# Performance work log

Measured on AMD Instinct MI355X. Metric: run time of the kernel, lower is better.

The kernel has to match this reference:

```python
import jax, jax.numpy as jnp
import numpy as np
from math import sqrt

S, B = 512, 64
V, E, H, T = 50000, 256, 512, 9
PAD = 0

def setup_inputs() -> dict:
    key = jax.random.key(0)
    ks = jax.random.split(key, 12)
    x = jax.random.randint(ks[0], (S, B), 0, V)
    x = x.at[0].set(jnp.maximum(x[0], 1))  # first token never pad (CRF mask req)
    bio = jax.random.randint(ks[1], (S, B), 0, T)
    sc = 0.02
    return {
        "x": x, "bio": bio,
        "emb": jax.random.normal(ks[2], (V, E), jnp.float32) * sc,
        "W_ih": jax.random.normal(ks[3], (4 * H, E), jnp.float32) * sc,
        "W_hh": jax.random.normal(ks[4], (4 * H, H), jnp.float32) * sc,
        "b_ih": jnp.zeros((4 * H,), jnp.float32),
        "b_hh": jnp.zeros((4 * H,), jnp.float32),
        "W_out": jax.random.normal(ks[5], (T, H), jnp.float32) * sc,
        "b_out": jnp.zeros((T,), jnp.float32),
        "start_t": jax.random.normal(ks[6], (T,), jnp.float32) * 0.1,
        "end_t": jax.random.normal(ks[7], (T,), jnp.float32) * 0.1,
        "trans": jax.random.normal(ks[8], (T, T), jnp.float32) * 0.1,
    }

def _lstm(embeds, W_ih, W_hh, b_ih, b_hh):
    # embeds: [S,B,E] time-major, single layer, pytorch gate order i,f,g,o
    def step(carry, e_t):
        h, c = carry
        gates = e_t @ W_ih.T + h @ W_hh.T + (b_ih + b_hh)  # [B,4H]
        i, f, g, o = jnp.split(gates, 4, axis=-1)
        i, f, o = jax.nn.sigmoid(i), jax.nn.sigmoid(f), jax.nn.sigmoid(o)
        c = f * c + i * jnp.tanh(g)
        h = o * jnp.tanh(c)
        return (h, c), h
    h0 = jnp.zeros((embeds.shape[1], W_hh.shape[1]), embeds.dtype)
    _, hs = jax.lax.scan(step, (h0, h0), embeds)
    return hs  # [S,B,H]

def _crf_llh(emissions, tags, maskf, start_t, end_t, trans):
    # emissions [S,B,T], tags [S,B], maskf [S,B] float. Returns summed log-likelihood.
    Bn = emissions.shape[1]
    barange = jnp.arange(Bn)
    em = jnp.take_along_axis(emissions, tags[:, :, None], axis=2)[:, :, 0]  # [S,B]
    tr = trans[tags[:-1], tags[1:]]  # [S-1,B]
    seq_ends = maskf.sum(0).astype(jnp.int32) - 1
    last_tags = tags[seq_ends, barange]
    num = (start_t[tags[0]] + em[0]
           + ((em[1:] + tr) * maskf[1:]).sum(0)
           + end_t[last_tags])  # [B]
    # normalizer: forward algorithm
    def step(score, inp):
        e_t, m_t = inp  # [B,T], [B]
        nxt = jax.nn.logsumexp(score[:, :, None] + trans[None] + e_t[:, None, :], axis=1)
        score = jnp.where(m_t[:, None] > 0, nxt, score)
        return score, None
    score0 = start_t[None] + emissions[0]  # [B,T]
    scoreN, _ = jax.lax.scan(step, score0, (emissions[1:], maskf[1:]))
    norm = jax.nn.logsumexp(scoreN + end_t[None], axis=1)  # [B]
    return (num - norm).sum()

def _viterbi(emissions, start_t, end_t, trans):
    # full-length decode (model calls crf.decode without mask)
    Bn, Tn = emissions.shape[1], emissions.shape[2]
    barange = jnp.arange(Bn)
    def step(score, e_t):
        cand = score[:, :, None] + trans[None]  # [B,T_prev,T_next]
        idx = jnp.argmax(cand, axis=1)          # [B,T]
        score = jnp.max(cand, axis=1) + e_t
        return score, idx
    score0 = start_t[None] + emissions[0]
    scoreN, history = jax.lax.scan(step, score0, emissions[1:])  # history [S-1,B,T]
    last = jnp.argmax(scoreN + end_t[None], axis=1)  # [B]
    def back(tag, h_t):
        prev = h_t[barange, tag]
        return prev, tag
    tag0, rest = jax.lax.scan(back, last, history, reverse=True)  # rest[t] = tag_{t+1}
    return jnp.concatenate([tag0[None], rest], axis=0)  # [S,B]

def reference(x, bio, emb, W_ih, W_hh, b_ih, b_hh, W_out, b_out, start_t, end_t, trans):
    maskf = (x != PAD).astype(jnp.float32)  # [S,B]
    embeds = emb[x] * sqrt(E)               # [S,B,E]
    lstm_out = _lstm(embeds, W_ih, W_hh, b_ih, b_hh)  # [S,B,H]
    logits = lstm_out @ W_out.T + b_out               # [S,B,T]
    emissions = jax.nn.log_softmax(logits, axis=-1)
    llh = _crf_llh(emissions, bio, maskf, start_t, end_t, trans)
    crf_tags = _viterbi(emissions, start_t, end_t, trans)
    return (-llh, crf_tags)
```

## Files before the change

kernel.cpp:

```cpp
#include <hip/hip_runtime.h>
#include <math.h>

#define SS 512
#define BB 64
#define EE 256
#define HH 512
#define NT 9
#define NWG 256

#define HS_ELEMS ((size_t)SS * BB * HH)
#define EM_OFF   HS_ELEMS
#define NUM_OFF  (EM_OFF + (size_t)SS * BB * NT)
#define NORM_OFF (NUM_OFF + 64)
#define FLAG_OFF (NORM_OFF + 64)
#define FLAG_U32S ((size_t)SS * 8 * 32)

#define L_WHH 0
#define L_H   32768
#define L_GSM 36928
#define L_CS  37504
#define L_TOT 37632

__global__ __launch_bounds__(256) void init_flags(float* __restrict__ ws) {
    unsigned* f = (unsigned*)(ws + FLAG_OFF);
    size_t idx = (size_t)blockIdx.x * 256 + threadIdx.x;
    if (idx < FLAG_U32S) f[idx] = 0u;
}

__global__ __launch_bounds__(512) void lstm_persistent(
    const float* __restrict__ Whh, const float* __restrict__ Wih,
    const float* __restrict__ bih, const float* __restrict__ bhh,
    const float* __restrict__ emb, const int* __restrict__ x,
    float* __restrict__ ws)
{
    const int wg    = blockIdx.x;
    const int slice = wg & 31;
    const int bg    = wg >> 5;
    const int tid   = threadIdx.x;
    const int w     = tid >> 6;
    const int L     = tid & 63;
    const int b_l   = L & 7;
    const int kc    = L >> 3;
    const int b     = bg * 8 + b_l;

    float* hs = ws;
    unsigned* flags = (unsigned*)(ws + FLAG_OFF);

    extern __shared__ float smem[];
    float* whh_l = smem + L_WHH;
    float* h_l   = smem + L_H;
    float* gsm   = smem + L_GSM;
    float* cs_l  = smem + L_CS;

    int grow[8];
#pragma unroll
    for (int r = 0; r < 8; r++) {
        int l = w * 8 + r;
        grow[r] = (l >> 4) * HH + slice * 16 + (l & 15);
    }

    for (int j = 0; j < 64; j++) {
        int idx = j * 512 + tid;
        int l = idx >> 9;
        int k = idx & 511;
        int gr = (l >> 4) * HH + slice * 16 + (l & 15);
        whh_l[idx] = Whh[(size_t)gr * HH + k];
    }

    float bs0 = 0.f, bs1 = 0.f, bs2 = 0.f, bs3 = 0.f;
    if (tid < 128) {
        const int u  = tid & 15;
        const int bb = tid >> 4;
        const int gu = slice * 16 + u;
        bs0 = bih[0 * HH + gu] + bhh[0 * HH + gu];
        bs1 = bih[1 * HH + gu] + bhh[1 * HH + gu];
        bs2 = bih[2 * HH + gu] + bhh[2 * HH + gu];
        bs3 = bih[3 * HH + gu] + bhh[3 * HH + gu];
        cs_l[u * 8 + bb] = 0.0f;
    }

#pragma unroll
    for (int j = 0; j < 8; j++) {
        int idx = j * 512 + tid;
        h_l[(idx >> 9) * 520 + (idx & 511)] = 0.0f;
    }

    float acc_ih[8];
    {
        const int xv = x[0 * BB + b];
        const float* erow = emb + (size_t)xv * EE;
#pragma unroll
        for (int r = 0; r < 8; r++) acc_ih[r] = 0.0f;
        for (int c = 0; c < 8; c++) {
            const int k0 = c * 32 + kc * 4;
            float4 e4 = *(const float4*)(erow + k0);
            e4.x *= 16.0f; e4.y *= 16.0f; e4.z *= 16.0f; e4.w *= 16.0f;
#pragma unroll
            for (int r = 0; r < 8; r++) {
                float4 w4 = *(const float4*)(Wih + (size_t)grow[r] * EE + k0);
                acc_ih[r] += w4.x * e4.x + w4.y * e4.y + w4.z * e4.z + w4.w * e4.w;
            }
        }
    }
    __syncthreads();

    const float* wbase = whh_l + (size_t)(w * 8) * 512;

    for (int t = 0; t < SS; t++) {
        float acc[8];
#pragma unroll
        for (int r = 0; r < 8; r++) acc[r] = acc_ih[r];
        const float* hrow = h_l + b_l * 520;
        for (int c = 0; c < 16; c++) {
            const int k0 = c * 32 + kc * 4;
            float4 h4 = *(const float4*)(hrow + k0);
#pragma unroll
            for (int r = 0; r < 8; r++) {
                float4 w4 = *(const float4*)(wbase + r * 512 + k0);
                acc[r] += w4.x * h4.x + w4.y * h4.y + w4.z * h4.z + w4.w * h4.w;
            }
        }

#pragma unroll
        for (int r = 0; r < 8; r++) {
            acc[r] += __shfl_xor(acc[r], 8, 64);
            acc[r] += __shfl_xor(acc[r], 16, 64);
            acc[r] += __shfl_xor(acc[r], 32, 64);
        }
        float myv = acc[0];
#pragma unroll
        for (int r = 1; r < 8; r++) if (kc == r) myv = acc[r];
        gsm[(w * 8 + kc) * 9 + b_l] = myv;
        __syncthreads();

        if (tid < 128) {
            const int u  = tid & 15;
            const int bb = tid >> 4;
            const int gu = slice * 16 + u;
            float gi = gsm[(0 * 16 + u) * 9 + bb] + bs0;
            float gf = gsm[(1 * 16 + u) * 9 + bb] + bs1;
            float gg = gsm[(2 * 16 + u) * 9 + bb] + bs2;
            float go = gsm[(3 * 16 + u) * 9 + bb] + bs3;
            float i_ = 1.0f / (1.0f + expf(-gi));
            float f_ = 1.0f / (1.0f + expf(-gf));
            float o_ = 1.0f / (1.0f + expf(-go));
            const int gb = bg * 8 + bb;
            float cn = f_ * cs_l[u * 8 + bb] + i_ * tanhf(gg);
            float hn = o_ * tanhf(cn);
            cs_l[u * 8 + bb] = cn;
            __hip_atomic_store(&hs[(size_t)t * BB * HH + (size_t)gb * HH + gu],
                               hn, __ATOMIC_RELAXED, __HIP_MEMORY_SCOPE_AGENT);
        }
        __syncthreads();

        if (t + 1 < SS) {
            if (tid == 0)
                __hip_atomic_store(&flags[((size_t)t * 8 + bg) * 32 + slice], 1u,
                                   __ATOMIC_RELAXED, __HIP_MEMORY_SCOPE_AGENT);

            {
                const int xv = x[(t + 1) * BB + b];
                const float* erow = emb + (size_t)xv * EE;
#pragma unroll
                for (int r = 0; r < 8; r++) acc_ih[r] = 0.0f;
                for (int c = 0; c < 8; c++) {
                    const int k0 = c * 32 + kc * 4;
                    float4 e4 = *(const float4*)(erow + k0);
                    e4.x *= 16.0f; e4.y *= 16.0f; e4.z *= 16.0f; e4.w *= 16.0f;
#pragma unroll
                    for (int r = 0; r < 8; r++) {
                        float4 w4 = *(const float4*)(Wih + (size_t)grow[r] * EE + k0);
                        acc_ih[r] += w4.x * e4.x + w4.y * e4.y + w4.z * e4.z + w4.w * e4.w;
                    }
                }
            }

            {
                const unsigned* fl = flags + ((size_t)t * 8 + bg) * 32;
                for (;;) {
                    unsigned v = 1u;
                    if (L < 32)
                        v = __hip_atomic_load(&fl[L], __ATOMIC_RELAXED,
                                              __HIP_MEMORY_SCOPE_AGENT);
                    if (__all(v != 0u)) break;
                }
            }

            const float* hsrc = hs + (size_t)t * BB * HH + (size_t)bg * 8 * HH;
#pragma unroll
            for (int j = 0; j < 8; j++) {
                int idx = j * 512 + tid;
                float v = __hip_atomic_load(&hsrc[idx], __ATOMIC_RELAXED,
                                            __HIP_MEMORY_SCOPE_AGENT);
                h_l[(idx >> 9) * 520 + (idx & 511)] = v;
            }
            __syncthreads();
        }
    }
}

__global__ __launch_bounds__(256) void emis_kernel(
    const float* __restrict__ Wout, const float* __restrict__ bout,
    float* __restrict__ ws)
{
    int wid = blockIdx.x * 4 + (threadIdx.x >> 6);
    int L   = threadIdx.x & 63;
    const float* h = ws + (size_t)wid * HH;
    float hv[8];
#pragma unroll
    for (int i = 0; i < 8; i++) hv[i] = h[i * 64 + L];
    float acc[9];
#pragma unroll
    for (int tg = 0; tg < 9; tg++) acc[tg] = 0.0f;
    for (int i = 0; i < 8; i++) {
#pragma unroll
        for (int tg = 0; tg < 9; tg++)
            acc[tg] += Wout[tg * HH + i * 64 + L] * hv[i];
    }
#pragma unroll
    for (int tg = 0; tg < 9; tg++) {
        acc[tg] += __shfl_xor(acc[tg], 1, 64);
        acc[tg] += __shfl_xor(acc[tg], 2, 64);
        acc[tg] += __shfl_xor(acc[tg], 4, 64);
        acc[tg] += __shfl_xor(acc[tg], 8, 64);
        acc[tg] += __shfl_xor(acc[tg], 16, 64);
        acc[tg] += __shfl_xor(acc[tg], 32, 64);
    }
    float lg[9];
#pragma unroll
    for (int tg = 0; tg < 9; tg++) lg[tg] = acc[tg] + bout[tg];
    float m = lg[0];
#pragma unroll
    for (int tg = 1; tg < 9; tg++) m = fmaxf(m, lg[tg]);
    float ssum = 0.0f;
#pragma unroll
    for (int tg = 0; tg < 9; tg++) ssum += expf(lg[tg] - m);
    float lse = m + logf(ssum);
    float myo = lg[0] - lse;
#pragma unroll
    for (int tg = 1; tg < 9; tg++) if (L == tg) myo = lg[tg] - lse;
    if (L < 9) ws[EM_OFF + (size_t)wid * 9 + L] = myo;
}

__global__ __launch_bounds__(512) void crf_all(
    const int* __restrict__ x, const int* __restrict__ bio,
    const float* __restrict__ start_t, const float* __restrict__ end_t,
    const float* __restrict__ trans, float* __restrict__ ws,
    float* __restrict__ out)
{
    const float* em = ws + EM_OFF;
    const int role  = blockIdx.x >> 3;
    const int local = blockIdx.x & 7;
    const int tid   = threadIdx.x;

    __shared__ float sc[9][8];
    __shared__ unsigned char hist[SS - 1][8][9];

    if (role == 0) {
        int b = local * 8 + (tid >> 6);
        int L = tid & 63;
        float sum = 0.0f;
        int cntm = 0;
#pragma unroll
        for (int j = 0; j < 8; j++) {
            int s = j * 64 + L;
            int tg = bio[s * BB + b];
            bool mk = (x[s * BB + b] != 0);
            cntm += mk ? 1 : 0;
            if (s == 0) {
                sum += start_t[tg] + em[(size_t)b * 9 + tg];
            } else if (mk) {
                int tp = bio[(s - 1) * BB + b];
                sum += em[((size_t)s * BB + b) * 9 + tg] + trans[tp * 9 + tg];
            }
        }
#pragma unroll
        for (int d = 1; d < 64; d <<= 1) {
            sum += __shfl_xor(sum, d, 64);
            cntm += __shfl_xor(cntm, d, 64);
        }
        if (L == 0) {
            int se = cntm - 1;
            sum += end_t[bio[se * BB + b]];
            ws[NUM_OFF + b] = sum;
        }
        return;
    }

    const int b_l = tid & 7;
    const int j   = tid >> 3;
    const int b   = local * 8 + b_l;
    float tc[9];
    if (j < 9) {
#pragma unroll
        for (int i = 0; i < 9; i++) tc[i] = trans[i * 9 + j];
        sc[j][b_l] = start_t[j] + em[(size_t)b * 9 + j];
    }
    __syncthreads();

    if (role == 1) {
        for (int s = 1; s < SS; s++) {
            float nv = 0.0f;
            if (j < 9) {
                float sv[9];
                float m = -3.4e38f;
#pragma unroll
                for (int i = 0; i < 9; i++) {
                    sv[i] = sc[i][b_l] + tc[i];
                    m = fmaxf(m, sv[i]);
                }
                float ssum = 0.0f;
#pragma unroll
                for (int i = 0; i < 9; i++) ssum += expf(sv[i] - m);
                nv = m + logf(ssum) + em[((size_t)s * BB + b) * 9 + j];
            }
            bool mk = (x[s * BB + b] != 0);
            __syncthreads();
            if (j < 9 && mk) sc[j][b_l] = nv;
            __syncthreads();
        }
        if (j == 0) {
            float m = -3.4e38f;
#pragma unroll
            for (int i = 0; i < 9; i++) m = fmaxf(m, sc[i][b_l] + end_t[i]);
            float ssum = 0.0f;
#pragma unroll
            for (int i = 0; i < 9; i++) ssum += expf(sc[i][b_l] + end_t[i] - m);
            ws[NORM_OFF + b] = m + logf(ssum);
        }
    } else {
        for (int s = 1; s < SS; s++) {
            float nv = 0.0f;
            if (j < 9) {
                float best = sc[0][b_l] + tc[0];
                int bi = 0;
#pragma unroll
                for (int i = 1; i < 9; i++) {
                    float v = sc[i][b_l] + tc[i];
                    if (v > best) { best = v; bi = i; }
                }
                hist[s - 1][b_l][j] = (unsigned char)bi;
                nv = best + em[((size_t)s * BB + b) * 9 + j];
            }
            __syncthreads();
            if (j < 9) sc[j][b_l] = nv;
            __syncthreads();
        }
        if (tid < 8) {
            int bl = tid;
            int gb = local * 8 + bl;
            float best = sc[0][bl] + end_t[0];
            int cur = 0;
#pragma unroll
            for (int i = 1; i < 9; i++) {
                float v = sc[i][bl] + end_t[i];
                if (v > best) { best = v; cur = i; }
            }
            out[1 + (size_t)(SS - 1) * BB + gb] = (float)cur;
            for (int s = SS - 2; s >= 0; s--) {
                cur = hist[s][bl][cur];
                out[1 + (size_t)s * BB + gb] = (float)cur;
            }
        }
    }
}

__global__ __launch_bounds__(64) void final_llh(const float* __restrict__ ws,
                                               float* __restrict__ out)
{
    int L = threadIdx.x;
    float v = ws[NUM_OFF + L] - ws[NORM_OFF + L];
    v += __shfl_xor(v, 1, 64);
    v += __shfl_xor(v, 2, 64);
    v += __shfl_xor(v, 4, 64);
    v += __shfl_xor(v, 8, 64);
    v += __shfl_xor(v, 16, 64);
    v += __shfl_xor(v, 32, 64);
    if (L == 0) out[0] = -v;
}

extern "C" void kernel_launch(void* const* d_in, const int* in_sizes, int n_in,
                              void* d_out, int out_size, void* d_ws, size_t ws_size,
                              hipStream_t stream) {
    const int*   x       = (const int*)d_in[0];
    const int*   bio     = (const int*)d_in[1];
    const float* emb     = (const float*)d_in[2];
    const float* W_ih    = (const float*)d_in[3];
    const float* W_hh    = (const float*)d_in[4];
    const float* b_ih    = (const float*)d_in[5];
    const float* b_hh    = (const float*)d_in[6];
    const float* W_out   = (const float*)d_in[7];
    const float* b_out   = (const float*)d_in[8];
    const float* start_t = (const float*)d_in[9];
    const float* end_t   = (const float*)d_in[10];
    const float* trans   = (const float*)d_in[11];
    float* out = (float*)d_out;
    float* ws  = (float*)d_ws;

    const size_t dyn_lds = (size_t)L_TOT * sizeof(float);
    hipFuncSetAttribute((const void*)lstm_persistent,
                        hipFuncAttributeMaxDynamicSharedMemorySize,
                        (int)dyn_lds);

    init_flags<<<512, 256, 0, stream>>>(ws);
    lstm_persistent<<<NWG, 512, dyn_lds, stream>>>(W_hh, W_ih, b_ih, b_hh, emb, x, ws);
    emis_kernel<<<SS * BB / 4, 256, 0, stream>>>(W_out, b_out, ws);
    crf_all<<<24, 512, 0, stream>>>(x, bio, start_t, end_t, trans, ws, out);
    final_llh<<<1, 64, 0, stream>>>(ws, out);
}
```

Before: 6.284 ms.

## Read previous hidden state directly from global memory, drop LDS staging barrier

Each wave now waits on the step flags itself and loads h_{t-1} straight from the global hs buffer with 64-bit atomic loads inside the recurrent dot product. This replaces the cooperative copy into LDS and the __syncthreads that followed it. The aim is to remove one block-wide barrier and an LDS round-trip per timestep on the serial critical path. In exchange, every wave polls the flags and re-reads the same hidden rows from L2, which adds global-memory latency inside the inner loop.

```diff
diff --git a/kernel.cpp b/kernel.cpp
--- a/kernel.cpp
+++ b/kernel.cpp
@@ -16,10 +16,9 @@
 #define FLAG_U32S ((size_t)SS * 8 * 32)
 
 #define L_WHH 0
-#define L_H   32768
-#define L_GSM 36928
-#define L_CS  37504
-#define L_TOT 37632
+#define L_GSM 32768
+#define L_CS  33344
+#define L_TOT 33472
 
 __global__ __launch_bounds__(256) void init_flags(float* __restrict__ ws) {
     unsigned* f = (unsigned*)(ws + FLAG_OFF);
@@ -48,7 +47,6 @@
 
     extern __shared__ float smem[];
     float* whh_l = smem + L_WHH;
-    float* h_l   = smem + L_H;
     float* gsm   = smem + L_GSM;
     float* cs_l  = smem + L_CS;
 
@@ -79,12 +77,6 @@
         cs_l[u * 8 + bb] = 0.0f;
     }
 
-#pragma unroll
-    for (int j = 0; j < 8; j++) {
-        int idx = j * 512 + tid;
-        h_l[(idx >> 9) * 520 + (idx & 511)] = 0.0f;
-    }
-
     float acc_ih[8];
     {
         const int xv = x[0 * BB + b];
@@ -110,14 +102,35 @@
         float acc[8];
 #pragma unroll
         for (int r = 0; r < 8; r++) acc[r] = acc_ih[r];
-        const float* hrow = h_l + b_l * 520;
-        for (int c = 0; c < 16; c++) {
-            const int k0 = c * 32 + kc * 4;
-            float4 h4 = *(const float4*)(hrow + k0);
-#pragma unroll
-            for (int r = 0; r < 8; r++) {
-                float4 w4 = *(const float4*)(wbase + r * 512 + k0);
-                acc[r] += w4.x * h4.x + w4.y * h4.y + w4.z * h4.z + w4.w * h4.w;
+
+        if (t > 0) {
+            const unsigned* fl = flags + ((size_t)(t - 1) * 8 + bg) * 32;
+            for (;;) {
+                unsigned v = 1u;
+                if (L < 32)
+                    v = __hip_atomic_load(&fl[L], __ATOMIC_RELAXED,
+                                          __HIP_MEMORY_SCOPE_AGENT);
+                if (__all(v != 0u)) break;
+            }
+
+            const float* hsrc = hs + (size_t)(t - 1) * BB * HH + (size_t)b * HH;
+            for (int c = 0; c < 16; c++) {
+                const int k0 = c * 32 + kc * 4;
+                unsigned long long u0 = __hip_atomic_load(
+                    (const unsigned long long*)(hsrc + k0),
+                    __ATOMIC_RELAXED, __HIP_MEMORY_SCOPE_AGENT);
+                unsigned long long u1 = __hip_atomic_load(
+                    (const unsigned long long*)(hsrc + k0 + 2),
+                    __ATOMIC_RELAXED, __HIP_MEMORY_SCOPE_AGENT);
+                float hx = __uint_as_float((unsigned)u0);
+                float hy = __uint_as_float((unsigned)(u0 >> 32));
+                float hz = __uint_as_float((unsigned)u1);
+                float hw = __uint_as_float((unsigned)(u1 >> 32));
+#pragma unroll
+                for (int r = 0; r < 8; r++) {
+                    float4 w4 = *(const float4*)(wbase + r * 512 + k0);
+                    acc[r] += w4.x * hx + w4.y * hy + w4.z * hz + w4.w * hw;
+                }
             }
         }
 
@@ -158,43 +171,20 @@
                 __hip_atomic_store(&flags[((size_t)t * 8 + bg) * 32 + slice], 1u,
                                    __ATOMIC_RELAXED, __HIP_MEMORY_SCOPE_AGENT);
 
-            {
-                const int xv = x[(t + 1) * BB + b];
-                const float* erow = emb + (size_t)xv * EE;
-#pragma unroll
-                for (int r = 0; r < 8; r++) acc_ih[r] = 0.0f;
-                for (int c = 0; c < 8; c++) {
-                    const int k0 = c * 32 + kc * 4;
-                    float4 e4 = *(const float4*)(erow + k0);
-                    e4.x *= 16.0f; e4.y *= 16.0f; e4.z *= 16.0f; e4.w *= 16.0f;
-#pragma unroll
-                    for (int r = 0; r < 8; r++) {
-                        float4 w4 = *(const float4*)(Wih + (size_t)grow[r] * EE + k0);
-                        acc_ih[r] += w4.x * e4.x + w4.y * e4.y + w4.z * e4.z + w4.w * e4.w;
-                    }
+            const int xv = x[(t + 1) * BB + b];
+            const float* erow = emb + (size_t)xv * EE;
+#pragma unroll
+            for (int r = 0; r < 8; r++) acc_ih[r] = 0.0f;
+            for (int c = 0; c < 8; c++) {
+                const int k0 = c * 32 + kc * 4;
+                float4 e4 = *(const float4*)(erow + k0);
+                e4.x *= 16.0f; e4.y *= 16.0f; e4.z *= 16.0f; e4.w *= 16.0f;
+#pragma unroll
+                for (int r = 0; r < 8; r++) {
+                    float4 w4 = *(const float4*)(Wih + (size_t)grow[r] * EE + k0);
+                    acc_ih[r] += w4.x * e4.x + w4.y * e4.y + w4.z * e4.z + w4.w * e4.w;
                 }
             }
-
-            {
-                const unsigned* fl = flags + ((size_t)t * 8 + bg) * 32;
-                for (;;) {
-                    unsigned v = 1u;
-                    if (L < 32)
-                        v = __hip_atomic_load(&fl[L], __ATOMIC_RELAXED,
-                                              __HIP_MEMORY_SCOPE_AGENT);
-                    if (__all(v != 0u)) break;
-                }
-            }
-
-            const float* hsrc = hs + (size_t)t * BB * HH + (size_t)bg * 8 * HH;
-#pragma unroll
-            for (int j = 0; j < 8; j++) {
-                int idx = j * 512 + tid;
-                float v = __hip_atomic_load(&hsrc[idx], __ATOMIC_RELAXED,
-                                            __HIP_MEMORY_SCOPE_AGENT);
-                h_l[(idx >> 9) * 520 + (idx & 511)] = v;
-            }
-            __syncthreads();
         }
     }
 }
```

Measured after the change: 8.308 ms. 32.2% more time.
